# Kernel optimization log

Hardware: AMD Instinct MI355X
Metric: run time of the kernel (lower is better)

The kernel has to match this reference:

```python
import jax, jax.numpy as jnp
import numpy as np

D_MODEL = 1024
N_HEAD = 16
D_K = D_MODEL // N_HEAD
B, S = 2, 2048


def setup_inputs() -> dict:
    key = jax.random.key(0)
    ks = jax.random.split(key, 12)
    sc = 1.0 / np.sqrt(D_MODEL)
    return {
        "q": jax.random.normal(ks[0], (B, S, D_MODEL), jnp.float32),
        "k": jax.random.normal(ks[1], (B, S, D_MODEL), jnp.float32),
        "v": jax.random.normal(ks[2], (B, S, D_MODEL), jnp.float32),
        "mask": jax.random.randint(ks[3], (B, S, S), 0, 2, jnp.int32),
        # learned params (torch Linear convention: y = x @ W + b with W pre-transposed)
        "wq": jax.random.normal(ks[4], (D_MODEL, D_MODEL), jnp.float32) * sc,
        "bq": jax.random.normal(ks[5], (D_MODEL,), jnp.float32) * sc,
        "wk": jax.random.normal(ks[6], (D_MODEL, D_MODEL), jnp.float32) * sc,  # no bias
        "wv": jax.random.normal(ks[7], (D_MODEL, D_MODEL), jnp.float32) * sc,
        "bv": jax.random.normal(ks[8], (D_MODEL,), jnp.float32) * sc,
        "wf": jax.random.normal(ks[9], (D_MODEL, D_MODEL), jnp.float32) * sc,
        "bf": jax.random.normal(ks[10], (D_MODEL,), jnp.float32) * sc,
    }


def reference(q, k, v, mask, wq, bq, wk, wv, bv, wf, bf):
    bs = q.shape[0]
    temperature = jnp.asarray(D_K ** 0.5, q.dtype)
    # projections -> [b, h, s, d_k]
    qh = (q @ wq + bq).reshape(bs, -1, N_HEAD, D_K).transpose(0, 2, 1, 3)
    kh = (k @ wk).reshape(bs, -1, N_HEAD, D_K).transpose(0, 2, 1, 3)
    vh = (v @ wv + bv).reshape(bs, -1, N_HEAD, D_K).transpose(0, 2, 1, 3)
    # scores [b, h, sq, sk]
    attn = jnp.einsum("bhqd,bhkd->bhqk", qh, kh) / temperature
    m0 = (mask[:, None, :, :] == 0)  # mask==0 -> masked out, broadcast over heads
    attn = jnp.where(m0, -jnp.inf, attn)
    attn = jax.nn.softmax(attn, axis=-1)
    attn = jnp.where(m0, 0.0, attn)
    out = jnp.einsum("bhqk,bhkd->bhqd", attn, vh)
    out = out.transpose(0, 2, 1, 3).reshape(bs, -1, D_MODEL)
    return out @ wf + bf  # dropout is identity in eval mode
```

## Files before the change

kernel.cpp:

```cpp
#include <hip/hip_runtime.h>

#define D_MODEL 1024
#define NHEAD   16
#define DK      64
#define BATCH   2
#define SEQ     2048

typedef __attribute__((ext_vector_type(8))) short bf16x8;
typedef __attribute__((ext_vector_type(4))) float f32x4;
typedef __attribute__((ext_vector_type(16))) float f32x16;
typedef __attribute__((ext_vector_type(4))) int i32x4;

#define QSCALE 0.18033688011f

__device__ __forceinline__ unsigned short f2b(float x) {
  unsigned u = __builtin_bit_cast(unsigned, x);
  u = (u + 0x7fffu + ((u >> 16) & 1u)) >> 16;
  return (unsigned short)u;
}
__device__ __forceinline__ unsigned short f2b_rhu(float x) {
  return (unsigned short)((__builtin_bit_cast(unsigned, x) + 0x8000u) >> 16);
}
__device__ __forceinline__ int pk2(float a, float b) {
  unsigned ua = __builtin_bit_cast(unsigned, a) + 0x8000u;
  unsigned ub = __builtin_bit_cast(unsigned, b) + 0x8000u;
  return (int)__builtin_amdgcn_perm(ub, ua, 0x07060302u);
}
__device__ __forceinline__ int pk2u(unsigned ua, unsigned ub) {
  return (int)__builtin_amdgcn_perm(ub + 0x8000u, ua + 0x8000u, 0x07060302u);
}

typedef const __attribute__((address_space(1))) void* gas_p;
typedef __attribute__((address_space(3))) void* las_p;
__device__ __forceinline__ void gll16(const void* g, void* l) {
  __builtin_amdgcn_global_load_lds((gas_p)g, (las_p)l, 16, 0, 0);
}

__device__ __forceinline__ f32x16 mfma32(bf16x8 a, bf16x8 b, f32x16 c) {
  return __builtin_amdgcn_mfma_f32_32x32x16_bf16(a, b, c, 0, 0, 0);
}

__global__ __launch_bounds__(256) void prep_kernel(
    const float* __restrict__ q, const float* __restrict__ k, const float* __restrict__ v,
    unsigned short* __restrict__ qb, unsigned short* __restrict__ kb,
    unsigned short* __restrict__ vb,
    const float* __restrict__ wq, const float* __restrict__ wk,
    const float* __restrict__ wv, const float* __restrict__ wf,
    unsigned short* __restrict__ wqt, unsigned short* __restrict__ wkt,
    unsigned short* __restrict__ wvt, unsigned short* __restrict__ wft,
    const int* __restrict__ mask, unsigned long long* __restrict__ mbits) {
  int bid = blockIdx.x, t = threadIdx.x;
  if (bid < 6144) {
    int by = bid >> 11, bx = bid & 2047;
    const float* src = by == 0 ? q : (by == 1 ? k : v);
    unsigned short* dst = by == 0 ? qb : (by == 1 ? kb : vb);
    size_t i = ((size_t)bx * 256 + t) * 8;
    float4 x0 = *(const float4*)&src[i];
    float4 x1 = *(const float4*)&src[i + 4];
    int4 w;
    w.x = pk2(x0.x, x0.y); w.y = pk2(x0.z, x0.w);
    w.z = pk2(x1.x, x1.y); w.w = pk2(x1.z, x1.w);
    *(int4*)&dst[i] = w;
  } else if (bid < 7168) {
    __shared__ float tile[64][65];
    int idx = bid - 6144;
    int bz = idx >> 8, by = (idx >> 4) & 15, bx = idx & 15;
    const float* w; unsigned short* wt;
    switch (bz) {
      case 0: w = wq; wt = wqt; break;
      case 1: w = wk; wt = wkt; break;
      case 2: w = wv; wt = wvt; break;
      default: w = wf; wt = wft; break;
    }
    int r0 = by * 64, c0 = bx * 64;
    for (int i = 0; i < 16; ++i) {
      int idx2 = t + i * 256; int r = idx2 >> 6, c = idx2 & 63;
      tile[r][c] = w[(size_t)(r0 + r) * D_MODEL + c0 + c];
    }
    __syncthreads();
    for (int i = 0; i < 16; ++i) {
      int idx2 = t + i * 256; int r = idx2 >> 6, c = idx2 & 63;
      wt[(size_t)(c0 + r) * D_MODEL + r0 + c] = f2b(tile[c][r]);
    }
  } else {
    int idx = bid - 7168;
    int lane = t & 63, wave = t >> 6;
    size_t base = ((size_t)idx * 4 + wave) * 256;
    unsigned long long b0 = __ballot(mask[base + lane] != 0);
    unsigned long long b1 = __ballot(mask[base + 64 + lane] != 0);
    unsigned long long b2 = __ballot(mask[base + 128 + lane] != 0);
    unsigned long long b3 = __ballot(mask[base + 192 + lane] != 0);
    if (lane == 0) {
      unsigned long long* p = &mbits[(size_t)idx * 16 + wave * 4];
      p[0] = b0; p[1] = b1; p[2] = b2; p[3] = b3;
    }
  }
}

__global__ __launch_bounds__(256) void gemm_qkv_kernel(
    const unsigned short* __restrict__ qb, const unsigned short* __restrict__ kb,
    const unsigned short* __restrict__ vb,
    const unsigned short* __restrict__ wqt, const unsigned short* __restrict__ wkt,
    const unsigned short* __restrict__ wvt,
    const float* __restrict__ bq, const float* __restrict__ bv,
    unsigned short* __restrict__ qh, unsigned short* __restrict__ kh,
    unsigned short* __restrict__ vt) {
  __shared__ unsigned short SB[16640];
  int bid = blockIdx.x;
  int xcd = bid & 7, slot = bid >> 3;
  int mi = slot & 3, zn = slot >> 2;
  int z = zn >> 3;
  int n0 = (zn & 7) * 128;
  int m0 = (mi * 8 + xcd) * 128;
  const unsigned short* A; const unsigned short* Bt;
  switch (z) {
    case 0:  A = qb; Bt = wqt; break;
    case 1:  A = kb; Bt = wkt; break;
    default: A = vb; Bt = wvt; break;
  }
  int t = threadIdx.x, lane = t & 63, wave = t >> 6;
  int l16 = lane & 15, quad = lane >> 4;
  int wm = (wave & 1) * 64, wn = (wave >> 1) * 64;
  f32x4 zero = {0.f, 0.f, 0.f, 0.f};
  f32x4 acc[4][4];
  for (int mt = 0; mt < 4; ++mt) for (int nt = 0; nt < 4; ++nt) acc[mt][nt] = zero;

  int drow = lane >> 2, dcol = (lane & 3) * 8;
  const unsigned short* asrc = A  + (size_t)(m0 + wave * 32 + drow) * D_MODEL + dcol;
  const unsigned short* bsrc = Bt + (size_t)(n0 + wave * 32 + drow) * D_MODEL + dcol;
  int dst = wave * 1024 + lane * 8;

#pragma unroll
  for (int g = 0; g < 2; ++g) {
    gll16(asrc + (size_t)(g * 16) * D_MODEL, &SB[dst + g * 512]);
    gll16(bsrc + (size_t)(g * 16) * D_MODEL, &SB[4096 + dst + g * 512]);
  }
  for (int it = 0; it < 32; ++it) {
    __syncthreads();
    if (it + 1 < 32) {
      int nb = ((it + 1) & 1) * 8192, kn = (it + 1) * 32;
#pragma unroll
      for (int g = 0; g < 2; ++g) {
        gll16(asrc + (size_t)(g * 16) * D_MODEL + kn, &SB[nb + dst + g * 512]);
        gll16(bsrc + (size_t)(g * 16) * D_MODEL + kn, &SB[nb + 4096 + dst + g * 512]);
      }
    }
    int cb = (it & 1) * 8192;
    bf16x8 a[4], b[4];
    for (int mt = 0; mt < 4; ++mt)
      a[mt] = *(const bf16x8*)&SB[cb + (wm + mt * 16 + l16) * 32 + quad * 8];
    for (int nt = 0; nt < 4; ++nt)
      b[nt] = *(const bf16x8*)&SB[cb + 4096 + (wn + nt * 16 + l16) * 32 + quad * 8];
    for (int mt = 0; mt < 4; ++mt)
      for (int nt = 0; nt < 4; ++nt)
        acc[mt][nt] = __builtin_amdgcn_mfma_f32_16x16x32_bf16(a[mt], b[nt], acc[mt][nt], 0, 0, 0);
  }

  if (z == 2) {
    __syncthreads();
    int qs = ((quad & 1) << 1) | (quad >> 1);
#pragma unroll
    for (int nt = 0; nt < 4; ++nt) {
      int col = wn + nt * 16 + l16;
      float bb = bv[n0 + col];
      for (int mt = 0; mt < 4; ++mt)
        for (int r = 0; r < 4; ++r)
          SB[col * 130 + wm + mt * 16 + qs * 4 + r] = f2b_rhu(acc[mt][nt][r] + bb);
    }
    __syncthreads();
    int c = t >> 1, hf = t & 1;
    int colg = n0 + c, hh = colg >> 6, dd = colg & 63;
    int b_ = m0 >> 11, sbase = m0 & (SEQ - 1);
    unsigned short* dstp = vt + (((size_t)(b_ * NHEAD + hh)) * DK + dd) * SEQ + sbase + hf * 64;
#pragma unroll
    for (int j = 0; j < 8; ++j)
      *(int4*)(dstp + j * 8) = *(const int4*)&SB[c * 130 + hf * 64 + j * 8];
  } else {
    __syncthreads();
#pragma unroll
    for (int nt = 0; nt < 4; ++nt) {
      int lcol = wn + nt * 16 + l16;
      float bb = (z == 0) ? bq[n0 + lcol] : 0.f;
      for (int mt = 0; mt < 4; ++mt)
        for (int r = 0; r < 4; ++r) {
          float val = acc[mt][nt][r] + bb;
          if (z == 0) val *= QSCALE;
          SB[(wm + mt * 16 + quad * 4 + r) * 130 + lcol] = f2b_rhu(val);
        }
    }
    __syncthreads();
    unsigned short* outp = (z == 0) ? qh : kh;
    int b_ = m0 >> 11, sbase = m0 & (SEQ - 1);
    int h0 = n0 >> 6, c = t & 7;
#pragma unroll
    for (int pass = 0; pass < 8; ++pass) {
      int rp = pass * 32 + (t >> 3);
      int srow = rp >> 1, part = rp & 1;
      unsigned short* dstp = outp +
          (((size_t)(b_ * NHEAD + h0 + part)) * SEQ + sbase + srow) * DK + c * 8;
      *(int4*)dstp = *(const int4*)&SB[srow * 130 + part * 64 + c * 8];
    }
  }
}

__global__ __launch_bounds__(256) void gemm_out_kernel(
    const unsigned short* __restrict__ A, const unsigned short* __restrict__ Bt,
    const float* __restrict__ bias, float* __restrict__ out) {
  __shared__ unsigned short As[8192], Bs[8192];
  int bid = blockIdx.x;
  int xcd = bid & 7, slot = bid >> 3;
  int mi = slot & 7, n0 = (slot >> 3) * 64;
  int m0 = (mi * 8 + xcd) * 64;
  int t = threadIdx.x, lane = t & 63, wave = t >> 6;
  int l16 = lane & 15, quad = lane >> 4;
  int wm = (wave & 1) * 32, wn = (wave >> 1) * 32;
  f32x4 zero = {0.f, 0.f, 0.f, 0.f};
  f32x4 acc[2][2];
  for (int mt = 0; mt < 2; ++mt) for (int nt = 0; nt < 2; ++nt) acc[mt][nt] = zero;

  int drow = lane >> 2, dcol = (lane & 3) * 8;
  const unsigned short* asrc = A  + (size_t)(m0 + wave * 16 + drow) * D_MODEL + dcol;
  const unsigned short* bsrc = Bt + (size_t)(n0 + wave * 16 + drow) * D_MODEL + dcol;
  int dst = wave * 512 + lane * 8;

#pragma unroll
  for (int hf = 0; hf < 2; ++hf) {
    gll16(asrc + hf * 32, &As[dst + hf * 2048]);
    gll16(bsrc + hf * 32, &Bs[dst + hf * 2048]);
  }
  for (int it = 0; it < 16; ++it) {
    __syncthreads();
    if (it + 1 < 16) {
      int nb = ((it + 1) & 1) * 4096, kn = (it + 1) * 64;
#pragma unroll
      for (int hf = 0; hf < 2; ++hf) {
        gll16(asrc + kn + hf * 32, &As[nb + dst + hf * 2048]);
        gll16(bsrc + kn + hf * 32, &Bs[nb + dst + hf * 2048]);
      }
    }
    int cb = (it & 1) * 4096;
#pragma unroll
    for (int half = 0; half < 2; ++half) {
      bf16x8 a[2], b[2];
      for (int mt = 0; mt < 2; ++mt)
        a[mt] = *(const bf16x8*)&As[cb + half * 2048 + (wm + mt * 16 + l16) * 32 + quad * 8];
      for (int nt = 0; nt < 2; ++nt)
        b[nt] = *(const bf16x8*)&Bs[cb + half * 2048 + (wn + nt * 16 + l16) * 32 + quad * 8];
      for (int mt = 0; mt < 2; ++mt)
        for (int nt = 0; nt < 2; ++nt)
          acc[mt][nt] = __builtin_amdgcn_mfma_f32_16x16x32_bf16(a[mt], b[nt], acc[mt][nt], 0, 0, 0);
    }
  }
  for (int nt = 0; nt < 2; ++nt) {
    int col = n0 + wn + nt * 16 + l16;
    float bb = bias[col];
    for (int mt = 0; mt < 2; ++mt)
      for (int r = 0; r < 4; ++r) {
        int row = m0 + wm + mt * 16 + quad * 4 + r;
        out[(size_t)row * D_MODEL + col] = acc[mt][nt][r] + bb;
      }
  }
}

__global__ __launch_bounds__(256, 2) void attn_kernel(
    const unsigned short* __restrict__ qh, const unsigned short* __restrict__ kh,
    const unsigned short* __restrict__ vt, const unsigned long long* __restrict__ mbits,
    unsigned short* __restrict__ attb) {
  __shared__ unsigned short Ks[16384];
  __shared__ unsigned short Vs[16384];
  int bid = blockIdx.x;
  int xcd = bid & 7, slot = bid >> 3;
  int bh_ = 4 * xcd + (slot >> 4);
  int qt = slot & 15;
  int b = bh_ >> 4, h = bh_ & 15;
  int t = threadIdx.x, lane = t & 63, wave = t >> 6;
  int l32 = lane & 31, hi = lane >> 5;
  size_t bh = (size_t)b * NHEAD + h;

  const unsigned short* Kg = kh + bh * SEQ * DK;
  const unsigned short* Vg = vt + bh * DK * SEQ;
  const unsigned long long* mrow = mbits + (size_t)b * SEQ * (SEQ / 64);
  int qrowb = qt * 128 + wave * 32;

  bf16x8 qf[4];
  {
    const unsigned short* Qg = qh + (bh * SEQ + (size_t)(qrowb + l32)) * DK;
#pragma unroll
    for (int step = 0; step < 4; ++step)
      qf[step] = *(const bf16x8*)&Qg[(step * 2 + hi) * 8];
  }

  int ksrow = t >> 3;
  int kschk = ((t & 7) ^ (ksrow & 7)) * 8;
  const unsigned short* ksrc = Kg + (size_t)ksrow * DK + kschk;
  int vsrow = t >> 4;
  int vschk = ((t & 15) ^ (vsrow & 15)) * 8;
  const unsigned short* vsrc = Vg + (size_t)vsrow * SEQ + vschk;
  int sdst = t * 8;

  int kx = l32 & 7;
  int kaddr[4];
#pragma unroll
  for (int step = 0; step < 4; ++step)
    kaddr[step] = l32 * 64 + (((step * 2 + hi) ^ kx) * 8);
  int vx = l32 & 15;

  size_t mi0 = (size_t)(qrowb + l32) * (SEQ / 64);

  bf16x8 ones8;
#pragma unroll
  for (int i = 0; i < 8; ++i) ones8[i] = (short)0x3F80;

  f32x16 zero16;
#pragma unroll
  for (int i = 0; i < 16; ++i) zero16[i] = 0.f;
  f32x16 accO0 = zero16, accO1 = zero16, accRS = zero16;

#pragma unroll
  for (int g = 0; g < 4; ++g) {
    gll16(ksrc + (size_t)(g * 32) * DK, &Ks[g * 2048 + sdst]);
    gll16(vsrc + (size_t)(g * 16) * SEQ, &Vs[g * 2048 + sdst]);
  }

  for (int tk = 0; tk < SEQ / 128; ++tk) {
    __syncthreads();
    if (tk + 1 < SEQ / 128) {
      int nb = ((tk + 1) & 1) * 8192;
      const unsigned short* kn = ksrc + (size_t)(tk + 1) * 128 * DK;
      const unsigned short* vn = vsrc + (tk + 1) * 128;
#pragma unroll
      for (int g = 0; g < 4; ++g) {
        gll16(kn + (size_t)(g * 32) * DK, &Ks[nb + g * 2048 + sdst]);
        gll16(vn + (size_t)(g * 16) * SEQ, &Vs[nb + g * 2048 + sdst]);
      }
    }
    unsigned long long m0 = mrow[mi0 + 2 * tk];
    unsigned long long m1 = mrow[mi0 + 2 * tk + 1];

    int cb = (tk & 1) * 8192;
#pragma unroll
    for (int kt = 0; kt < 4; ++kt) {
      f32x16 accS = zero16;
      __builtin_amdgcn_s_setprio(1);
#pragma unroll
      for (int step = 0; step < 4; ++step) {
        bf16x8 kf = *(const bf16x8*)&Ks[cb + kt * 2048 + kaddr[step]];
        accS = mfma32(kf, qf[step], accS);
      }
      __builtin_amdgcn_s_setprio(0);

      unsigned wk_ = (unsigned)(((kt < 2) ? m0 : m1) >> ((kt & 1) * 32));
      unsigned w = wk_ >> (4 * hi);
      unsigned pu[16];
#pragma unroll
      for (int r = 0; r < 16; ++r) {
        float pv = __builtin_amdgcn_exp2f(accS[r]);
        const int pos = (r & 3) + 8 * (r >> 2);
        int msk = ((int)(w << (31 - pos))) >> 31;
        pu[r] = __builtin_bit_cast(unsigned, pv) & (unsigned)msk;
      }
      i32x4 w0v = {pk2u(pu[0], pu[1]),  pk2u(pu[2], pu[3]),
                   pk2u(pu[4], pu[5]),  pk2u(pu[6], pu[7])};
      i32x4 w1v = {pk2u(pu[8], pu[9]),  pk2u(pu[10], pu[11]),
                   pk2u(pu[12], pu[13]), pk2u(pu[14], pu[15])};
      bf16x8 ap0 = __builtin_bit_cast(bf16x8, w0v);
      bf16x8 ap1 = __builtin_bit_cast(bf16x8, w1v);

      __builtin_amdgcn_s_setprio(1);
      accRS = mfma32(ap0, ones8, accRS);
      accRS = mfma32(ap1, ones8, accRS);
      {
        int c0 = ((kt * 4 + hi) ^ vx) * 8;
        int c1 = ((kt * 4 + 2 + hi) ^ vx) * 8;
        bf16x8 vf00 = *(const bf16x8*)&Vs[cb + l32 * 128 + c0];
        bf16x8 vf01 = *(const bf16x8*)&Vs[cb + 4096 + l32 * 128 + c0];
        bf16x8 vf10 = *(const bf16x8*)&Vs[cb + l32 * 128 + c1];
        bf16x8 vf11 = *(const bf16x8*)&Vs[cb + 4096 + l32 * 128 + c1];
        accO0 = mfma32(ap0, vf00, accO0);
        accO1 = mfma32(ap0, vf01, accO1);
        accO0 = mfma32(ap1, vf10, accO0);
        accO1 = mfma32(ap1, vf11, accO1);
      }
      __builtin_amdgcn_s_setprio(0);
    }
  }

#pragma unroll
  for (int r = 0; r < 16; ++r) {
    float sden = accRS[r];
    float inv = sden > 0.f ? 1.f / sden : 0.f;
    int qq = (r & 3) + 8 * (r >> 2) + 4 * hi;
    int row = qrowb + qq;
    size_t ob = ((size_t)b * SEQ + row) * D_MODEL + (size_t)h * DK + l32;
    attb[ob] = f2b_rhu(accO0[r] * inv);
    attb[ob + 32] = f2b_rhu(accO1[r] * inv);
  }
}

extern "C" void kernel_launch(void* const* d_in, const int* in_sizes, int n_in,
                              void* d_out, int out_size, void* d_ws, size_t ws_size,
                              hipStream_t stream) {
  (void)in_sizes; (void)n_in; (void)out_size; (void)ws_size;
  const float* q    = (const float*)d_in[0];
  const float* k    = (const float*)d_in[1];
  const float* v    = (const float*)d_in[2];
  const int*   mask = (const int*)d_in[3];
  const float* wq   = (const float*)d_in[4];
  const float* bq   = (const float*)d_in[5];
  const float* wk   = (const float*)d_in[6];
  const float* wv   = (const float*)d_in[7];
  const float* bv   = (const float*)d_in[8];
  const float* wf   = (const float*)d_in[9];
  const float* bf   = (const float*)d_in[10];

  char* ws = (char*)d_ws;
  unsigned short* wft  = (unsigned short*)(ws + 0);
  unsigned short* wqt  = (unsigned short*)(ws + 2097152);
  unsigned short* wkt  = (unsigned short*)(ws + 4194304);
  unsigned short* wvt  = (unsigned short*)(ws + 6291456);
  unsigned short* attb = (unsigned short*)(ws + 2097152);
  unsigned short* qhp  = (unsigned short*)(ws + 10485760);
  unsigned short* khp  = (unsigned short*)(ws + 18874368);
  unsigned short* vtp  = (unsigned short*)(ws + 27262976);
  unsigned long long* mbits = (unsigned long long*)(ws + 35651584);
  unsigned short* vb   = (unsigned short*)(ws + 36700160);
  unsigned short* qb   = (unsigned short*)d_out;
  unsigned short* kb   = (unsigned short*)d_out + 4194304;

  hipLaunchKernelGGL(prep_kernel, dim3(15360), dim3(256), 0, stream,
                     q, k, v, qb, kb, vb,
                     wq, wk, wv, wf, wqt, wkt, wvt, wft, mask, mbits);
  hipLaunchKernelGGL(gemm_qkv_kernel, dim3(768), dim3(256), 0, stream,
                     qb, kb, vb, wqt, wkt, wvt, bq, bv, qhp, khp, vtp);
  hipLaunchKernelGGL(attn_kernel, dim3(512), dim3(256), 0, stream,
                     qhp, khp, vtp, mbits, attb);
  hipLaunchKernelGGL(gemm_out_kernel, dim3(1024), dim3(256), 0, stream,
                     attb, wft, bf, (float*)d_out);
}
```

Baseline: 255.9 us.

## Split attention key range across two wave groups with LDS reduction

The attention kernel goes from 4 to 8 waves per block. The two wave groups each process half of every 128-key tile for the same 128 query rows. The per-group output and row-sum accumulators are then combined through shared memory before normalisation and the store. This is meant to raise occupancy and latency hiding within each block, at the cost of an extra reduction, two more barriers, and a changed K/V LDS staging layout.

```diff
diff --git a/kernel.cpp b/kernel.cpp
--- a/kernel.cpp
+++ b/kernel.cpp
@@ -262,7 +262,7 @@
   }
 }
 
-__global__ __launch_bounds__(256, 2) void attn_kernel(
+__global__ __launch_bounds__(512, 4) void attn_kernel(
     const unsigned short* __restrict__ qh, const unsigned short* __restrict__ kh,
     const unsigned short* __restrict__ vt, const unsigned long long* __restrict__ mbits,
     unsigned short* __restrict__ attb) {
@@ -274,13 +274,14 @@
   int qt = slot & 15;
   int b = bh_ >> 4, h = bh_ & 15;
   int t = threadIdx.x, lane = t & 63, wave = t >> 6;
+  int qsub = wave & 3, grp = wave >> 2;
   int l32 = lane & 31, hi = lane >> 5;
   size_t bh = (size_t)b * NHEAD + h;
 
   const unsigned short* Kg = kh + bh * SEQ * DK;
   const unsigned short* Vg = vt + bh * DK * SEQ;
   const unsigned long long* mrow = mbits + (size_t)b * SEQ * (SEQ / 64);
-  int qrowb = qt * 128 + wave * 32;
+  int qrowb = qt * 128 + qsub * 32;
 
   bf16x8 qf[4];
   {
@@ -290,12 +291,10 @@
       qf[step] = *(const bf16x8*)&Qg[(step * 2 + hi) * 8];
   }
 
-  int ksrow = t >> 3;
-  int kschk = ((t & 7) ^ (ksrow & 7)) * 8;
-  const unsigned short* ksrc = Kg + (size_t)ksrow * DK + kschk;
-  int vsrow = t >> 4;
-  int vschk = ((t & 15) ^ (vsrow & 15)) * 8;
-  const unsigned short* vsrc = Vg + (size_t)vsrow * SEQ + vschk;
+  int srow = t >> 3;
+  int schk = ((t & 7) ^ (srow & 7)) * 8;
+  const unsigned short* kbase = Kg + (size_t)srow * DK + schk;
+  const unsigned short* vbase = Vg + (size_t)srow * SEQ + schk;
   int sdst = t * 8;
 
   int kx = l32 & 7;
@@ -303,7 +302,6 @@
 #pragma unroll
   for (int step = 0; step < 4; ++step)
     kaddr[step] = l32 * 64 + (((step * 2 + hi) ^ kx) * 8);
-  int vx = l32 & 15;
 
   size_t mi0 = (size_t)(qrowb + l32) * (SEQ / 64);
 
@@ -316,41 +314,37 @@
   for (int i = 0; i < 16; ++i) zero16[i] = 0.f;
   f32x16 accO0 = zero16, accO1 = zero16, accRS = zero16;
 
-#pragma unroll
-  for (int g = 0; g < 4; ++g) {
-    gll16(ksrc + (size_t)(g * 32) * DK, &Ks[g * 2048 + sdst]);
-    gll16(vsrc + (size_t)(g * 16) * SEQ, &Vs[g * 2048 + sdst]);
-  }
-
-  for (int tk = 0; tk < SEQ / 128; ++tk) {
-    __syncthreads();
-    if (tk + 1 < SEQ / 128) {
-      int nb = ((tk + 1) & 1) * 8192;
-      const unsigned short* kn = ksrc + (size_t)(tk + 1) * 128 * DK;
-      const unsigned short* vn = vsrc + (tk + 1) * 128;
-#pragma unroll
-      for (int g = 0; g < 4; ++g) {
-        gll16(kn + (size_t)(g * 32) * DK, &Ks[nb + g * 2048 + sdst]);
-        gll16(vn + (size_t)(g * 16) * SEQ, &Vs[nb + g * 2048 + sdst]);
-      }
-    }
-    unsigned long long m0 = mrow[mi0 + 2 * tk];
-    unsigned long long m1 = mrow[mi0 + 2 * tk + 1];
-
-    int cb = (tk & 1) * 8192;
-#pragma unroll
-    for (int kt = 0; kt < 4; ++kt) {
+  gll16(kbase, &Ks[sdst]);
+  gll16(kbase + (size_t)64 * DK, &Ks[4096 + sdst]);
+  gll16(vbase, &Vs[sdst]);
+  gll16(vbase + 64, &Vs[4096 + sdst]);
+
+  for (int tr = 0; tr < SEQ / 128; ++tr) {
+    __syncthreads();
+    if (tr + 1 < SEQ / 128) {
+      int nb = ((tr + 1) & 1) * 8192;
+      size_t k0 = (size_t)(tr + 1) * 128;
+      gll16(kbase + k0 * DK, &Ks[nb + sdst]);
+      gll16(kbase + (k0 + 64) * DK, &Ks[nb + 4096 + sdst]);
+      gll16(vbase + k0, &Vs[nb + sdst]);
+      gll16(vbase + k0 + 64, &Vs[nb + 4096 + sdst]);
+    }
+    unsigned long long mw = mrow[mi0 + 2 * tr + grp];
+
+    int tb = (tr & 1) * 8192 + grp * 4096;
+
+#pragma unroll
+    for (int kt2 = 0; kt2 < 2; ++kt2) {
       f32x16 accS = zero16;
       __builtin_amdgcn_s_setprio(1);
 #pragma unroll
       for (int step = 0; step < 4; ++step) {
-        bf16x8 kf = *(const bf16x8*)&Ks[cb + kt * 2048 + kaddr[step]];
+        bf16x8 kf = *(const bf16x8*)&Ks[tb + kt2 * 2048 + kaddr[step]];
         accS = mfma32(kf, qf[step], accS);
       }
       __builtin_amdgcn_s_setprio(0);
 
-      unsigned wk_ = (unsigned)(((kt < 2) ? m0 : m1) >> ((kt & 1) * 32));
-      unsigned w = wk_ >> (4 * hi);
+      unsigned w = (unsigned)(mw >> (kt2 * 32)) >> (4 * hi);
       unsigned pu[16];
 #pragma unroll
       for (int r = 0; r < 16; ++r) {
@@ -370,12 +364,12 @@
       accRS = mfma32(ap0, ones8, accRS);
       accRS = mfma32(ap1, ones8, accRS);
       {
-        int c0 = ((kt * 4 + hi) ^ vx) * 8;
-        int c1 = ((kt * 4 + 2 + hi) ^ vx) * 8;
-        bf16x8 vf00 = *(const bf16x8*)&Vs[cb + l32 * 128 + c0];
-        bf16x8 vf01 = *(const bf16x8*)&Vs[cb + 4096 + l32 * 128 + c0];
-        bf16x8 vf10 = *(const bf16x8*)&Vs[cb + l32 * 128 + c1];
-        bf16x8 vf11 = *(const bf16x8*)&Vs[cb + 4096 + l32 * 128 + c1];
+        int c0 = ((kt2 * 4 + hi) ^ kx) * 8;
+        int c1 = ((kt2 * 4 + 2 + hi) ^ kx) * 8;
+        bf16x8 vf00 = *(const bf16x8*)&Vs[tb + l32 * 64 + c0];
+        bf16x8 vf01 = *(const bf16x8*)&Vs[tb + 2048 + l32 * 64 + c0];
+        bf16x8 vf10 = *(const bf16x8*)&Vs[tb + l32 * 64 + c1];
+        bf16x8 vf11 = *(const bf16x8*)&Vs[tb + 2048 + l32 * 64 + c1];
         accO0 = mfma32(ap0, vf00, accO0);
         accO1 = mfma32(ap0, vf01, accO1);
         accO0 = mfma32(ap1, vf10, accO0);
@@ -385,15 +379,41 @@
     }
   }
 
-#pragma unroll
-  for (int r = 0; r < 16; ++r) {
-    float sden = accRS[r];
-    float inv = sden > 0.f ? 1.f / sden : 0.f;
-    int qq = (r & 3) + 8 * (r >> 2) + 4 * hi;
-    int row = qrowb + qq;
-    size_t ob = ((size_t)b * SEQ + row) * D_MODEL + (size_t)h * DK + l32;
-    attb[ob] = f2b_rhu(accO0[r] * inv);
-    attb[ob + 32] = f2b_rhu(accO1[r] * inv);
+  __syncthreads();
+  if (grp == 1) {
+    float* redO = (float*)Ks;
+    float* redR = (float*)Vs;
+    int ro = (qsub * 64 + lane) * 32;
+    int rr = (qsub * 64 + lane) * 16;
+#pragma unroll
+    for (int r = 0; r < 16; ++r) {
+      redO[ro + r] = accO0[r];
+      redO[ro + 16 + r] = accO1[r];
+      redR[rr + r] = accRS[r];
+    }
+  }
+  __syncthreads();
+  if (grp == 0) {
+    const float* redO = (const float*)Ks;
+    const float* redR = (const float*)Vs;
+    int ro = (qsub * 64 + lane) * 32;
+    int rr = (qsub * 64 + lane) * 16;
+#pragma unroll
+    for (int r = 0; r < 16; ++r) {
+      accO0[r] += redO[ro + r];
+      accO1[r] += redO[ro + 16 + r];
+      accRS[r] += redR[rr + r];
+    }
+#pragma unroll
+    for (int r = 0; r < 16; ++r) {
+      float sden = accRS[r];
+      float inv = sden > 0.f ? 1.f / sden : 0.f;
+      int qq = (r & 3) + 8 * (r >> 2) + 4 * hi;
+      int row = qrowb + qq;
+      size_t ob = ((size_t)b * SEQ + row) * D_MODEL + (size_t)h * DK + l32;
+      attb[ob] = f2b_rhu(accO0[r] * inv);
+      attb[ob + 32] = f2b_rhu(accO1[r] * inv);
+    }
   }
 }
 
@@ -432,7 +452,7 @@
                      wq, wk, wv, wf, wqt, wkt, wvt, wft, mask, mbits);
   hipLaunchKernelGGL(gemm_qkv_kernel, dim3(768), dim3(256), 0, stream,
                      qb, kb, vb, wqt, wkt, wvt, bq, bv, qhp, khp, vtp);
-  hipLaunchKernelGGL(attn_kernel, dim3(512), dim3(256), 0, stream,
+  hipLaunchKernelGGL(attn_kernel, dim3(512), dim3(512), 0, stream,
                      qhp, khp, vtp, mbits, attb);
   hipLaunchKernelGGL(gemm_out_kernel, dim3(1024), dim3(256), 0, stream,
                      attb, wft, bf, (float*)d_out);
```

Result: faster. 247.2 us (-3.4%).

## Retile output GEMM to 128x64, stage epilogue in LDS, prefetch mask bits

Applied to the files above, without the earlier changes.

The output-projection GEMM now uses 128x64 block tiles with a K step of 32, which halves the grid to 512 blocks. Each wave computes 64x32, so every loaded B fragment is reused across more rows. The epilogue writes the accumulators plus bias into LDS and then stores coalesced float4 rows instead of scattered scalar stores. The attention kernel fetches the mask words for the next key tile one iteration early, hiding global load latency behind the MFMA work. In exchange the GEMM uses more registers and LDS, needs twice as many K iterations with a barrier each, and launches fewer blocks, which may leave CUs less full.

```diff
diff --git a/kernel.cpp b/kernel.cpp
--- a/kernel.cpp
+++ b/kernel.cpp
@@ -206,59 +206,71 @@
 __global__ __launch_bounds__(256) void gemm_out_kernel(
     const unsigned short* __restrict__ A, const unsigned short* __restrict__ Bt,
     const float* __restrict__ bias, float* __restrict__ out) {
-  __shared__ unsigned short As[8192], Bs[8192];
+  __shared__ __align__(16) char SMEM[34816];
+  unsigned short* As = (unsigned short*)SMEM;
+  unsigned short* Bs = (unsigned short*)SMEM + 8192;
+  float* OS = (float*)SMEM;
   int bid = blockIdx.x;
   int xcd = bid & 7, slot = bid >> 3;
-  int mi = slot & 7, n0 = (slot >> 3) * 64;
-  int m0 = (mi * 8 + xcd) * 64;
+  int mi = slot & 3, ni = slot >> 2;
+  int m0 = (mi * 8 + xcd) * 128, n0 = ni * 64;
   int t = threadIdx.x, lane = t & 63, wave = t >> 6;
   int l16 = lane & 15, quad = lane >> 4;
-  int wm = (wave & 1) * 32, wn = (wave >> 1) * 32;
+  int wm = (wave & 1) * 64, wn = (wave >> 1) * 32;
   f32x4 zero = {0.f, 0.f, 0.f, 0.f};
-  f32x4 acc[2][2];
-  for (int mt = 0; mt < 2; ++mt) for (int nt = 0; nt < 2; ++nt) acc[mt][nt] = zero;
+  f32x4 acc[4][2];
+  for (int mt = 0; mt < 4; ++mt) for (int nt = 0; nt < 2; ++nt) acc[mt][nt] = zero;
 
   int drow = lane >> 2, dcol = (lane & 3) * 8;
-  const unsigned short* asrc = A  + (size_t)(m0 + wave * 16 + drow) * D_MODEL + dcol;
-  const unsigned short* bsrc = Bt + (size_t)(n0 + wave * 16 + drow) * D_MODEL + dcol;
-  int dst = wave * 512 + lane * 8;
-
-#pragma unroll
-  for (int hf = 0; hf < 2; ++hf) {
-    gll16(asrc + hf * 32, &As[dst + hf * 2048]);
-    gll16(bsrc + hf * 32, &Bs[dst + hf * 2048]);
-  }
-  for (int it = 0; it < 16; ++it) {
-    __syncthreads();
-    if (it + 1 < 16) {
-      int nb = ((it + 1) & 1) * 4096, kn = (it + 1) * 64;
-#pragma unroll
-      for (int hf = 0; hf < 2; ++hf) {
-        gll16(asrc + kn + hf * 32, &As[nb + dst + hf * 2048]);
-        gll16(bsrc + kn + hf * 32, &Bs[nb + dst + hf * 2048]);
-      }
-    }
-    int cb = (it & 1) * 4096;
-#pragma unroll
-    for (int half = 0; half < 2; ++half) {
-      bf16x8 a[2], b[2];
-      for (int mt = 0; mt < 2; ++mt)
-        a[mt] = *(const bf16x8*)&As[cb + half * 2048 + (wm + mt * 16 + l16) * 32 + quad * 8];
+  const unsigned short* asrc = A  + (size_t)(m0 + wave * 32 + drow) * D_MODEL + dcol;
+  const unsigned short* bsrc = Bt + (size_t)(n0 + (t >> 2)) * D_MODEL + (t & 3) * 8;
+  int adst = wave * 1024 + lane * 8;
+  int bdst = t * 8;
+
+#pragma unroll
+  for (int g = 0; g < 2; ++g)
+    gll16(asrc + (size_t)(g * 16) * D_MODEL, &As[adst + g * 512]);
+  gll16(bsrc, &Bs[bdst]);
+
+  for (int it = 0; it < 32; ++it) {
+    __syncthreads();
+    if (it + 1 < 32) {
+      int na = ((it + 1) & 1) * 4096, nbb = ((it + 1) & 1) * 2048;
+      int kn = (it + 1) * 32;
+#pragma unroll
+      for (int g = 0; g < 2; ++g)
+        gll16(asrc + (size_t)(g * 16) * D_MODEL + kn, &As[na + adst + g * 512]);
+      gll16(bsrc + kn, &Bs[nbb + bdst]);
+    }
+    int ca = (it & 1) * 4096, cbb = (it & 1) * 2048;
+    bf16x8 a[4], b[2];
+    for (int mt = 0; mt < 4; ++mt)
+      a[mt] = *(const bf16x8*)&As[ca + (wm + mt * 16 + l16) * 32 + quad * 8];
+    for (int nt = 0; nt < 2; ++nt)
+      b[nt] = *(const bf16x8*)&Bs[cbb + (wn + nt * 16 + l16) * 32 + quad * 8];
+    for (int mt = 0; mt < 4; ++mt)
       for (int nt = 0; nt < 2; ++nt)
-        b[nt] = *(const bf16x8*)&Bs[cb + half * 2048 + (wn + nt * 16 + l16) * 32 + quad * 8];
-      for (int mt = 0; mt < 2; ++mt)
-        for (int nt = 0; nt < 2; ++nt)
-          acc[mt][nt] = __builtin_amdgcn_mfma_f32_16x16x32_bf16(a[mt], b[nt], acc[mt][nt], 0, 0, 0);
-    }
-  }
-  for (int nt = 0; nt < 2; ++nt) {
-    int col = n0 + wn + nt * 16 + l16;
-    float bb = bias[col];
-    for (int mt = 0; mt < 2; ++mt)
-      for (int r = 0; r < 4; ++r) {
-        int row = m0 + wm + mt * 16 + quad * 4 + r;
-        out[(size_t)row * D_MODEL + col] = acc[mt][nt][r] + bb;
-      }
+        acc[mt][nt] = __builtin_amdgcn_mfma_f32_16x16x32_bf16(a[mt], b[nt], acc[mt][nt], 0, 0, 0);
+  }
+
+  __syncthreads();
+  {
+    float b0 = bias[n0 + wn + l16];
+    float b1 = bias[n0 + wn + 16 + l16];
+#pragma unroll
+    for (int mt = 0; mt < 4; ++mt)
+      for (int nt = 0; nt < 2; ++nt)
+        for (int r = 0; r < 4; ++r)
+          OS[(wm + mt * 16 + quad * 4 + r) * 68 + wn + nt * 16 + l16] =
+              acc[mt][nt][r] + (nt ? b1 : b0);
+  }
+  __syncthreads();
+#pragma unroll
+  for (int pass = 0; pass < 8; ++pass) {
+    int row = pass * 16 + (t >> 4);
+    int c4 = (t & 15) * 4;
+    *(float4*)&out[(size_t)(m0 + row) * D_MODEL + n0 + c4] =
+        *(const float4*)&OS[row * 68 + c4];
   }
 }
 
@@ -282,6 +294,10 @@
   const unsigned long long* mrow = mbits + (size_t)b * SEQ * (SEQ / 64);
   int qrowb = qt * 128 + wave * 32;
 
+  size_t mi0 = (size_t)(qrowb + l32) * (SEQ / 64);
+  unsigned long long m0 = mrow[mi0];
+  unsigned long long m1 = mrow[mi0 + 1];
+
   bf16x8 qf[4];
   {
     const unsigned short* Qg = qh + (bh * SEQ + (size_t)(qrowb + l32)) * DK;
@@ -305,8 +321,6 @@
     kaddr[step] = l32 * 64 + (((step * 2 + hi) ^ kx) * 8);
   int vx = l32 & 15;
 
-  size_t mi0 = (size_t)(qrowb + l32) * (SEQ / 64);
-
   bf16x8 ones8;
 #pragma unroll
   for (int i = 0; i < 8; ++i) ones8[i] = (short)0x3F80;
@@ -324,6 +338,7 @@
 
   for (int tk = 0; tk < SEQ / 128; ++tk) {
     __syncthreads();
+    unsigned long long n0m = m0, n1m = m1;
     if (tk + 1 < SEQ / 128) {
       int nb = ((tk + 1) & 1) * 8192;
       const unsigned short* kn = ksrc + (size_t)(tk + 1) * 128 * DK;
@@ -333,9 +348,9 @@
         gll16(kn + (size_t)(g * 32) * DK, &Ks[nb + g * 2048 + sdst]);
         gll16(vn + (size_t)(g * 16) * SEQ, &Vs[nb + g * 2048 + sdst]);
       }
-    }
-    unsigned long long m0 = mrow[mi0 + 2 * tk];
-    unsigned long long m1 = mrow[mi0 + 2 * tk + 1];
+      n0m = mrow[mi0 + 2 * (tk + 1)];
+      n1m = mrow[mi0 + 2 * (tk + 1) + 1];
+    }
 
     int cb = (tk & 1) * 8192;
 #pragma unroll
@@ -383,6 +398,7 @@
       }
       __builtin_amdgcn_s_setprio(0);
     }
+    m0 = n0m; m1 = n1m;
   }
 
 #pragma unroll
@@ -434,6 +450,6 @@
                      qb, kb, vb, wqt, wkt, wvt, bq, bv, qhp, khp, vtp);
   hipLaunchKernelGGL(attn_kernel, dim3(512), dim3(256), 0, stream,
                      qhp, khp, vtp, mbits, attb);
-  hipLaunchKernelGGL(gemm_out_kernel, dim3(1024), dim3(256), 0, stream,
+  hipLaunchKernelGGL(gemm_out_kernel, dim3(512), dim3(256), 0, stream,
                      attb, wft, bf, (float*)d_out);
 }
```

After: 248.6 us. 1.03x faster.
